# Optimization experiments

Measured on AMD Instinct MI355X. Metric: run time of the kernel, lower is better.

The kernel has to match this reference:

```python
import jax, jax.numpy as jnp
import numpy as np

D_MODEL = 2048
NUM_HEADS = 32
NUM_GROUPS = 8
D_K = D_MODEL // NUM_HEADS          # 64
GROUP_SIZE = NUM_HEADS // NUM_GROUPS  # 4


def setup_inputs() -> dict:
    key = jax.random.key(0)
    ks = jax.random.split(key, 7)
    B, S = 2, 2048
    x = jax.random.normal(ks[0], (B, S, D_MODEL), dtype=jnp.float32)
    sc = 1.0 / np.sqrt(D_MODEL)
    Wq = jax.random.normal(ks[1], (D_MODEL, D_MODEL), dtype=jnp.float32) * sc
    bq = jax.random.normal(ks[2], (D_MODEL,), dtype=jnp.float32) * 0.01
    Wk = jax.random.normal(ks[3], (D_MODEL, D_K * NUM_GROUPS), dtype=jnp.float32) * sc
    bk = jax.random.normal(ks[4], (D_K * NUM_GROUPS,), dtype=jnp.float32) * 0.01
    Wv = jax.random.normal(ks[5], (D_MODEL, D_K * NUM_GROUPS), dtype=jnp.float32) * sc
    bv = jax.random.normal(ks[6], (D_K * NUM_GROUPS,), dtype=jnp.float32) * 0.01
    return {"x": x, "Wq": Wq, "bq": bq, "Wk": Wk, "bk": bk, "Wv": Wv, "bv": bv}


def reference(x, Wq, bq, Wk, bk, Wv, bv):
    B, S, D = x.shape
    # q: (B, G, gs, S, dk)
    q = (x @ Wq + bq).reshape(B, S, NUM_HEADS, D_K).transpose(0, 2, 1, 3)
    q = q.reshape(B, NUM_GROUPS, GROUP_SIZE, S, D_K)
    # k, v: (B, G, S, dk)
    k = (x @ Wk + bk).reshape(B, S, NUM_GROUPS, D_K).transpose(0, 2, 1, 3)
    v = (x @ Wv + bv).reshape(B, S, NUM_GROUPS, D_K).transpose(0, 2, 1, 3)
    # scores: (B, G, gs, S_q, S_k)
    scores = jnp.einsum('bgqsd,bgtd->bgqst', q, k) / (D_K ** 0.5)
    attn = jax.nn.softmax(scores, axis=-1)
    out = jnp.einsum('bgqst,bgtd->bgqsd', attn, v)  # (B, G, gs, S, dk)
    # Faithful to source: transpose(1,2) then view(B, S, -1) (scrambles seq axis)
    out = out.transpose(0, 2, 1, 3, 4).reshape(B, S, -1)
    return out
```

## Files before the change

### kernel.cpp

```cpp
#include <hip/hip_runtime.h>

typedef _Float16 f16;
typedef _Float16 half8 __attribute__((ext_vector_type(8)));
typedef _Float16 half4v __attribute__((ext_vector_type(4)));
typedef __fp16 fp16x2 __attribute__((ext_vector_type(2)));
typedef float floatx4 __attribute__((ext_vector_type(4)));
typedef float f32x16 __attribute__((ext_vector_type(16)));
typedef unsigned uint4v __attribute__((ext_vector_type(4)));

#define GLL16(g, l) __builtin_amdgcn_global_load_lds( \
    (const __attribute__((address_space(1))) void*)(g), \
    (__attribute__((address_space(3))) void*)(l), 16, 0, 0)

static __device__ __forceinline__ float pairsum(float x) {
    return x + __shfl_xor(x, 32);
}
static __device__ __forceinline__ unsigned pkh(float a, float b) {
    fp16x2 h = __builtin_amdgcn_cvt_pkrtz(a, b);
    return __builtin_bit_cast(unsigned, h);
}

__global__ __launch_bounds__(256) void cvt_x_kernel(const float* __restrict__ x,
                                                    f16* __restrict__ xh) {
    size_t i = ((size_t)blockIdx.x * 256 + threadIdx.x) * 8;
    float4 a = *(const float4*)(x + i);
    float4 b = *(const float4*)(x + i + 4);
    half8 h;
    h[0] = (f16)a.x; h[1] = (f16)a.y; h[2] = (f16)a.z; h[3] = (f16)a.w;
    h[4] = (f16)b.x; h[5] = (f16)b.y; h[6] = (f16)b.z; h[7] = (f16)b.w;
    *(half8*)(xh + i) = h;
}

__global__ __launch_bounds__(256) void wt_kernel(const float* __restrict__ Wq,
                                                 const float* __restrict__ Wk,
                                                 const float* __restrict__ Wv,
                                                 f16* __restrict__ Wt) {
    __shared__ float tile[64][65];
    int n0 = (blockIdx.x % 48) * 64;
    int k0 = (blockIdx.x / 48) * 64;
    const float* src; int ld, c0;
    if (n0 < 2048)      { src = Wq; ld = 2048; c0 = n0; }
    else if (n0 < 2560) { src = Wk; ld = 512;  c0 = n0 - 2048; }
    else                { src = Wv; ld = 512;  c0 = n0 - 2560; }
    int t = threadIdx.x;
    #pragma unroll
    for (int i = 0; i < 16; ++i) {
        int idx = t + i * 256;
        int r = idx >> 6, c = idx & 63;
        tile[r][c] = src[(size_t)(k0 + r) * ld + c0 + c];
    }
    __syncthreads();
    #pragma unroll
    for (int i = 0; i < 2; ++i) {
        int idx = t + i * 256;
        int nr = idx >> 3, kc = (idx & 7) * 8;
        half8 h;
        #pragma unroll
        for (int j = 0; j < 8; ++j) h[j] = (f16)tile[kc + j][nr];
        *(half8*)(Wt + (size_t)(n0 + nr) * 2048 + k0 + kc) = h;
    }
}

__global__ __launch_bounds__(256) void qkv_gemm_kernel(
    const f16* __restrict__ A, const f16* __restrict__ Bt,
    const float* __restrict__ bq, const float* __restrict__ bk, const float* __restrict__ bv,
    f16* __restrict__ Qb, f16* __restrict__ Kb, f16* __restrict__ Vt) {
    __shared__ f16 As[128 * 64];
    __shared__ f16 Bs[128 * 64];
    const int K = 2048;
    int bid = blockIdx.x;
    int j5 = bid >> 3;
    int tm = (bid & 7) + 8 * (j5 / 24);
    int tn = j5 % 24;
    int m0 = tm * 128, n0 = tn * 128;
    int tid = threadIdx.x, lane = tid & 63, wid = tid >> 6;
    int wr = wid >> 1, wc = wid & 1;
    int lr = lane & 15, lg = lane >> 4;
    floatx4 acc[4][4] = {};

    int lrow = wid * 8 + (lane >> 3);
    int lcol = (((lane & 7) ^ ((lane >> 3) & 7)) * 8);
    char* AsB = (char*)As;
    char* BsB = (char*)Bs;
    int rsw = (lr & 7) << 4;

    for (int kt = 0; kt < K; kt += 64) {
        __syncthreads();
        #pragma unroll
        for (int i = 0; i < 4; ++i) {
            GLL16(A  + (size_t)(m0 + i * 32 + lrow) * K + kt + lcol, AsB + i * 4096 + wid * 1024);
            GLL16(Bt + (size_t)(n0 + i * 32 + lrow) * K + kt + lcol, BsB + i * 4096 + wid * 1024);
        }
        __syncthreads();
        #pragma unroll
        for (int ks = 0; ks < 2; ++ks) {
            half8 af[4], bf[4];
            #pragma unroll
            for (int i = 0; i < 4; ++i)
                af[i] = *(const half8*)(AsB + (wr * 64 + i * 16 + lr) * 128 + ((ks * 64 + lg * 16) ^ rsw));
            #pragma unroll
            for (int i = 0; i < 4; ++i)
                bf[i] = *(const half8*)(BsB + (wc * 64 + i * 16 + lr) * 128 + ((ks * 64 + lg * 16) ^ rsw));
            #pragma unroll
            for (int i = 0; i < 4; ++i)
                #pragma unroll
                for (int jj = 0; jj < 4; ++jj)
                    acc[i][jj] = __builtin_amdgcn_mfma_f32_16x16x32_f16(bf[jj], af[i], acc[i][jj], 0, 0, 0);
        }
    }

    int b = m0 >> 11;
    #pragma unroll
    for (int jj = 0; jj < 4; ++jj) {
        int nb = n0 + wc * 64 + jj * 16 + lg * 4;
        if (nb < 2048) {
            int hcol = nb >> 6, d0 = nb & 63;
            float4 bias4 = *(const float4*)(bq + nb);
            f16* dstb = Qb + (size_t)(b * 32 + hcol) * 131072 + d0;
            #pragma unroll
            for (int i = 0; i < 4; ++i) {
                int s = (m0 + wr * 64 + i * 16 + lr) & 2047;
                half4v hv;
                hv[0] = (f16)(acc[i][jj][0] + bias4.x);
                hv[1] = (f16)(acc[i][jj][1] + bias4.y);
                hv[2] = (f16)(acc[i][jj][2] + bias4.z);
                hv[3] = (f16)(acc[i][jj][3] + bias4.w);
                *(half4v*)(dstb + (size_t)s * 64) = hv;
            }
        } else if (nb < 2560) {
            int nk = nb - 2048;
            int gg = nk >> 6, d0 = nk & 63;
            float4 bias4 = *(const float4*)(bk + nk);
            f16* dstb = Kb + (size_t)(b * 8 + gg) * 131072 + d0;
            #pragma unroll
            for (int i = 0; i < 4; ++i) {
                int s = (m0 + wr * 64 + i * 16 + lr) & 2047;
                half4v hv;
                hv[0] = (f16)(acc[i][jj][0] + bias4.x);
                hv[1] = (f16)(acc[i][jj][1] + bias4.y);
                hv[2] = (f16)(acc[i][jj][2] + bias4.z);
                hv[3] = (f16)(acc[i][jj][3] + bias4.w);
                *(half4v*)(dstb + (size_t)s * 64) = hv;
            }
        } else {
            int nv = nb - 2560;
            int gg = nv >> 6, d0 = nv & 63;
            float4 bias4 = *(const float4*)(bv + nv);
            f16* dstb = Vt + (size_t)((b * 8 + gg) * 64 + d0) * 2048;
            #pragma unroll
            for (int i = 0; i < 4; ++i) {
                int s = (m0 + wr * 64 + i * 16 + lr) & 2047;
                int sp = (s & ~12) | ((s & 4) << 1) | ((s & 8) >> 1);
                dstb[sp]            = (f16)(acc[i][jj][0] + bias4.x);
                dstb[2048 + sp]     = (f16)(acc[i][jj][1] + bias4.y);
                dstb[4096 + sp]     = (f16)(acc[i][jj][2] + bias4.z);
                dstb[6144 + sp]     = (f16)(acc[i][jj][3] + bias4.w);
            }
        }
    }
}

__global__ __launch_bounds__(128, 2) void attn_kernel(
    const f16* __restrict__ Qb, const f16* __restrict__ Kb, const f16* __restrict__ Vt,
    float* __restrict__ out) {
    __shared__ __align__(16) f16 Kl[2][64 * 64];
    __shared__ __align__(16) f16 Vl[2][64 * 64];

    int bid = blockIdx.x;
    int hh = (bid & 7) * 8 + ((bid >> 3) & 7);
    int qb = bid >> 6;
    int b = hh >> 5, h = hh & 31, g = h >> 2, qh = h & 3;
    int tid = threadIdx.x, lane = tid & 63, wid = tid >> 6;
    int lc = lane & 31, hi = lane >> 5;

    const f16* Qhead = Qb + (size_t)(b * 32 + h) * 131072;
    const f16* Khead = Kb + (size_t)(b * 8 + g) * 131072;
    const f16* Vhead = Vt + (size_t)(b * 8 + g) * 131072;
    int q0 = qb * 128 + wid * 64;
    int sqA = q0 + lc, sqB = q0 + 32 + lc;

    half8 qfA[4], qfB[4];
    #pragma unroll
    for (int ks = 0; ks < 4; ++ks) {
        qfA[ks] = *(const half8*)(Qhead + (size_t)sqA * 64 + ks * 16 + hi * 8);
        qfB[ks] = *(const half8*)(Qhead + (size_t)sqB * 64 + ks * 16 + hi * 8);
    }

    f32x16 ocA0 = {}, ocA1 = {}, ocB0 = {}, ocB1 = {};
    float lA = 0.f, lB = 0.f;
    const float SC = 0.125f * 1.44269504088896f;
    const float MSH = 5.770780163555851f;

    int r_ = wid * 32 + (lane >> 3);
    int csx = ((lane & 7) ^ (r_ & 7)) * 8;
    char* KlB = (char*)Kl;
    char* VlB = (char*)Vl;

    int ro0 = lc * 128, ro1 = (lc + 32) * 128;
    int sw = (lc & 7) << 4;

    #pragma unroll
    for (int i = 0; i < 4; ++i) {
        GLL16(Khead + (size_t)(r_ + i * 8) * 64 + csx,        KlB + wid * 4096 + i * 1024);
        GLL16(Vhead + (size_t)(r_ + i * 8) * 2048 + csx,      VlB + wid * 4096 + i * 1024);
    }
    __syncthreads();

    #pragma unroll 1
    for (int t = 0; t < 32; ++t) {
        int c = t & 1;
        char* KB = KlB + c * 8192;
        char* VB = VlB + c * 8192;
        if (t < 31) {
            int nk = (t + 1) * 64;
            #pragma unroll
            for (int i = 0; i < 4; ++i) {
                GLL16(Khead + (size_t)(nk + r_ + i * 8) * 64 + csx,
                      KlB + (c ^ 1) * 8192 + wid * 4096 + i * 1024);
                GLL16(Vhead + (size_t)(r_ + i * 8) * 2048 + nk + csx,
                      VlB + (c ^ 1) * 8192 + wid * 4096 + i * 1024);
            }
        }

        f32x16 sA0 = {}, sA1 = {}, sB0 = {}, sB1 = {};
        __builtin_amdgcn_s_setprio(1);
        #pragma unroll
        for (int ks = 0; ks < 4; ++ks) {
            half8 kf0 = *(const half8*)(KB + ((ro0 + ks * 32 + hi * 16) ^ sw));
            half8 kf1 = *(const half8*)(KB + ((ro1 + ks * 32 + hi * 16) ^ sw));
            sA0 = __builtin_amdgcn_mfma_f32_32x32x16_f16(kf0, qfA[ks], sA0, 0, 0, 0);
            sA1 = __builtin_amdgcn_mfma_f32_32x32x16_f16(kf1, qfA[ks], sA1, 0, 0, 0);
            sB0 = __builtin_amdgcn_mfma_f32_32x32x16_f16(kf0, qfB[ks], sB0, 0, 0, 0);
            sB1 = __builtin_amdgcn_mfma_f32_32x32x16_f16(kf1, qfB[ks], sB1, 0, 0, 0);
        }
        __builtin_amdgcn_s_setprio(0);

        float rsA = 0.f, rsB = 0.f;
        #pragma unroll
        for (int r = 0; r < 16; ++r) {
            float pa0 = __builtin_amdgcn_exp2f(fmaf(sA0[r], SC, -MSH));
            float pa1 = __builtin_amdgcn_exp2f(fmaf(sA1[r], SC, -MSH));
            float pb0 = __builtin_amdgcn_exp2f(fmaf(sB0[r], SC, -MSH));
            float pb1 = __builtin_amdgcn_exp2f(fmaf(sB1[r], SC, -MSH));
            sA0[r] = pa0; sA1[r] = pa1; sB0[r] = pb0; sB1[r] = pb1;
            rsA += pa0 + pa1; rsB += pb0 + pb1;
        }
        lA += rsA; lB += rsB;

        #pragma unroll
        for (int tt = 0; tt < 2; ++tt) {
            #pragma unroll
            for (int ks2 = 0; ks2 < 2; ++ks2) {
                int base = ks2 * 8;
                uint4v uA, uB;
                if (tt == 0) {
                    uA[0] = pkh(sA0[base + 0], sA0[base + 1]);
                    uA[1] = pkh(sA0[base + 2], sA0[base + 3]);
                    uA[2] = pkh(sA0[base + 4], sA0[base + 5]);
                    uA[3] = pkh(sA0[base + 6], sA0[base + 7]);
                    uB[0] = pkh(sB0[base + 0], sB0[base + 1]);
                    uB[1] = pkh(sB0[base + 2], sB0[base + 3]);
                    uB[2] = pkh(sB0[base + 4], sB0[base + 5]);
                    uB[3] = pkh(sB0[base + 6], sB0[base + 7]);
                } else {
                    uA[0] = pkh(sA1[base + 0], sA1[base + 1]);
                    uA[1] = pkh(sA1[base + 2], sA1[base + 3]);
                    uA[2] = pkh(sA1[base + 4], sA1[base + 5]);
                    uA[3] = pkh(sA1[base + 6], sA1[base + 7]);
                    uB[0] = pkh(sB1[base + 0], sB1[base + 1]);
                    uB[1] = pkh(sB1[base + 2], sB1[base + 3]);
                    uB[2] = pkh(sB1[base + 4], sB1[base + 5]);
                    uB[3] = pkh(sB1[base + 6], sB1[base + 7]);
                }
                half8 pA = __builtin_bit_cast(half8, uA);
                half8 pB = __builtin_bit_cast(half8, uB);
                int cb = tt * 64 + ks2 * 32 + hi * 16;
                half8 vf0 = *(const half8*)(VB + ((ro0 + cb) ^ sw));
                half8 vf1 = *(const half8*)(VB + ((ro1 + cb) ^ sw));
                __builtin_amdgcn_s_setprio(1);
                ocA0 = __builtin_amdgcn_mfma_f32_32x32x16_f16(vf0, pA, ocA0, 0, 0, 0);
                ocA1 = __builtin_amdgcn_mfma_f32_32x32x16_f16(vf1, pA, ocA1, 0, 0, 0);
                ocB0 = __builtin_amdgcn_mfma_f32_32x32x16_f16(vf0, pB, ocB0, 0, 0, 0);
                ocB1 = __builtin_amdgcn_mfma_f32_32x32x16_f16(vf1, pB, ocB1, 0, 0, 0);
                __builtin_amdgcn_s_setprio(0);
            }
        }
        __syncthreads();
    }

    lA = pairsum(lA); lB = pairsum(lB);
    float invA = 1.f / lA, invB = 1.f / lB;
    size_t obase = (size_t)b * 4194304 + (size_t)(qh * 8 + g) * 131072 + hi * 4;
    size_t obA = obase + (size_t)sqA * 64;
    size_t obB = obase + (size_t)sqB * 64;
    #pragma unroll
    for (int rg = 0; rg < 4; ++rg) {
        floatx4 vA0, vA1, vB0, vB1;
        #pragma unroll
        for (int j = 0; j < 4; ++j) {
            vA0[j] = ocA0[rg * 4 + j] * invA;
            vA1[j] = ocA1[rg * 4 + j] * invA;
            vB0[j] = ocB0[rg * 4 + j] * invB;
            vB1[j] = ocB1[rg * 4 + j] * invB;
        }
        *(floatx4*)(out + obA + rg * 8) = vA0;
        *(floatx4*)(out + obA + 32 + rg * 8) = vA1;
        *(floatx4*)(out + obB + rg * 8) = vB0;
        *(floatx4*)(out + obB + 32 + rg * 8) = vB1;
    }
}

extern "C" void kernel_launch(void* const* d_in, const int* in_sizes, int n_in,
                              void* d_out, int out_size, void* d_ws, size_t ws_size,
                              hipStream_t stream) {
    const float* x  = (const float*)d_in[0];
    const float* Wq = (const float*)d_in[1];
    const float* bq = (const float*)d_in[2];
    const float* Wk = (const float*)d_in[3];
    const float* bk = (const float*)d_in[4];
    const float* Wv = (const float*)d_in[5];
    const float* bv = (const float*)d_in[6];
    float* out = (float*)d_out;

    char* ws = (char*)d_ws;
    f16* xh = (f16*)ws;
    f16* Wt = (f16*)(ws + 16777216);
    f16* Qb = (f16*)(ws + 29360128);
    f16* Kb = (f16*)(ws + 46137344);
    f16* Vt = (f16*)(ws + 50331648);

    cvt_x_kernel<<<4096, 256, 0, stream>>>(x, xh);
    wt_kernel<<<1536, 256, 0, stream>>>(Wq, Wk, Wv, Wt);
    qkv_gemm_kernel<<<768, 256, 0, stream>>>(xh, Wt, bq, bk, bv, Qb, Kb, Vt);
    attn_kernel<<<1024, 128, 0, stream>>>(Qb, Kb, Vt, out);
}
```

Baseline: 184.9 us.

## Software-pipeline attention: overlap next-tile QK MFMA with current softmax and PV

Restructures the attention main loop so the QK^T scores for tile t+1 are computed while tile t's softmax and P·V run, with K triple-buffered in LDS and prefetched two tiles ahead. The loop is unrolled by two and alternates between two score register sets. The aim is to hide exp/pack VALU latency behind MFMA work. The cost is extra registers for a second 64-value score set and extra LDS, which at 2 waves-per-EU launch bounds could cause spilling or lower occupancy.

```diff
diff --git a/kernel.cpp b/kernel.cpp
--- a/kernel.cpp
+++ b/kernel.cpp
@@ -18,6 +18,9 @@
 static __device__ __forceinline__ unsigned pkh(float a, float b) {
     fp16x2 h = __builtin_amdgcn_cvt_pkrtz(a, b);
     return __builtin_bit_cast(unsigned, h);
+}
+static __device__ __forceinline__ f32x16 mf(half8 a, half8 b, f32x16 c) {
+    return __builtin_amdgcn_mfma_f32_32x32x16_f16(a, b, c, 0, 0, 0);
 }
 
 __global__ __launch_bounds__(256) void cvt_x_kernel(const float* __restrict__ x,
@@ -160,10 +163,93 @@
     }
 }
 
+typedef struct { f32x16 a0, a1, b0, b1; } SS;
+
+static __device__ __forceinline__ void qk_step(const char* kR, int ro0, int ro1,
+        int sw, int hi, const half8 qfA[4], const half8 qfB[4], SS& S) {
+    f32x16 z = {};
+    S.a0 = z; S.a1 = z; S.b0 = z; S.b1 = z;
+    #pragma unroll
+    for (int ks = 0; ks < 4; ++ks) {
+        half8 kf0 = *(const half8*)(kR + ((ro0 + ks * 32 + hi * 16) ^ sw));
+        half8 kf1 = *(const half8*)(kR + ((ro1 + ks * 32 + hi * 16) ^ sw));
+        S.a0 = mf(kf0, qfA[ks], S.a0);
+        S.a1 = mf(kf1, qfA[ks], S.a1);
+        S.b0 = mf(kf0, qfB[ks], S.b0);
+        S.b1 = mf(kf1, qfB[ks], S.b1);
+    }
+}
+
+static __device__ __forceinline__ void sm_pack(SS& S, float& lA, float& lB,
+                                               uint4v PA[4], uint4v PB[4]) {
+    const float SC = 0.125f * 1.44269504088896f;
+    const float MSH = 5.770780163555851f;
+    float rsA = 0.f, rsB = 0.f;
+    #pragma unroll
+    for (int r = 0; r < 16; ++r) {
+        float a0 = __builtin_amdgcn_exp2f(fmaf(S.a0[r], SC, -MSH));
+        float a1 = __builtin_amdgcn_exp2f(fmaf(S.a1[r], SC, -MSH));
+        float b0 = __builtin_amdgcn_exp2f(fmaf(S.b0[r], SC, -MSH));
+        float b1 = __builtin_amdgcn_exp2f(fmaf(S.b1[r], SC, -MSH));
+        S.a0[r] = a0; S.a1[r] = a1; S.b0[r] = b0; S.b1[r] = b1;
+        rsA += a0 + a1; rsB += b0 + b1;
+    }
+    lA += rsA; lB += rsB;
+    #pragma unroll
+    for (int tt = 0; tt < 2; ++tt) {
+        #pragma unroll
+        for (int ks2 = 0; ks2 < 2; ++ks2) {
+            int base = ks2 * 8;
+            uint4v uA, uB;
+            if (tt == 0) {
+                uA[0] = pkh(S.a0[base + 0], S.a0[base + 1]);
+                uA[1] = pkh(S.a0[base + 2], S.a0[base + 3]);
+                uA[2] = pkh(S.a0[base + 4], S.a0[base + 5]);
+                uA[3] = pkh(S.a0[base + 6], S.a0[base + 7]);
+                uB[0] = pkh(S.b0[base + 0], S.b0[base + 1]);
+                uB[1] = pkh(S.b0[base + 2], S.b0[base + 3]);
+                uB[2] = pkh(S.b0[base + 4], S.b0[base + 5]);
+                uB[3] = pkh(S.b0[base + 6], S.b0[base + 7]);
+            } else {
+                uA[0] = pkh(S.a1[base + 0], S.a1[base + 1]);
+                uA[1] = pkh(S.a1[base + 2], S.a1[base + 3]);
+                uA[2] = pkh(S.a1[base + 4], S.a1[base + 5]);
+                uA[3] = pkh(S.a1[base + 6], S.a1[base + 7]);
+                uB[0] = pkh(S.b1[base + 0], S.b1[base + 1]);
+                uB[1] = pkh(S.b1[base + 2], S.b1[base + 3]);
+                uB[2] = pkh(S.b1[base + 4], S.b1[base + 5]);
+                uB[3] = pkh(S.b1[base + 6], S.b1[base + 7]);
+            }
+            PA[tt * 2 + ks2] = uA;
+            PB[tt * 2 + ks2] = uB;
+        }
+    }
+}
+
+static __device__ __forceinline__ void pv_step(const char* vR, int ro0, int ro1,
+        int sw, int hi, const uint4v PA[4], const uint4v PB[4],
+        f32x16& oA0, f32x16& oA1, f32x16& oB0, f32x16& oB1) {
+    #pragma unroll
+    for (int tt = 0; tt < 2; ++tt) {
+        #pragma unroll
+        for (int ks2 = 0; ks2 < 2; ++ks2) {
+            int cb = tt * 64 + ks2 * 32 + hi * 16;
+            half8 vf0 = *(const half8*)(vR + ((ro0 + cb) ^ sw));
+            half8 vf1 = *(const half8*)(vR + ((ro1 + cb) ^ sw));
+            half8 pA = __builtin_bit_cast(half8, PA[tt * 2 + ks2]);
+            half8 pB = __builtin_bit_cast(half8, PB[tt * 2 + ks2]);
+            oA0 = mf(vf0, pA, oA0);
+            oA1 = mf(vf1, pA, oA1);
+            oB0 = mf(vf0, pB, oB0);
+            oB1 = mf(vf1, pB, oB1);
+        }
+    }
+}
+
 __global__ __launch_bounds__(128, 2) void attn_kernel(
     const f16* __restrict__ Qb, const f16* __restrict__ Kb, const f16* __restrict__ Vt,
     float* __restrict__ out) {
-    __shared__ __align__(16) f16 Kl[2][64 * 64];
+    __shared__ __align__(16) f16 Kl[3][64 * 64];
     __shared__ __align__(16) f16 Vl[2][64 * 64];
 
     int bid = blockIdx.x;
@@ -188,105 +274,61 @@
 
     f32x16 ocA0 = {}, ocA1 = {}, ocB0 = {}, ocB1 = {};
     float lA = 0.f, lB = 0.f;
-    const float SC = 0.125f * 1.44269504088896f;
-    const float MSH = 5.770780163555851f;
 
     int r_ = wid * 32 + (lane >> 3);
     int csx = ((lane & 7) ^ (r_ & 7)) * 8;
     char* KlB = (char*)Kl;
     char* VlB = (char*)Vl;
-
     int ro0 = lc * 128, ro1 = (lc + 32) * 128;
     int sw = (lc & 7) << 4;
 
     #pragma unroll
     for (int i = 0; i < 4; ++i) {
-        GLL16(Khead + (size_t)(r_ + i * 8) * 64 + csx,        KlB + wid * 4096 + i * 1024);
-        GLL16(Vhead + (size_t)(r_ + i * 8) * 2048 + csx,      VlB + wid * 4096 + i * 1024);
+        GLL16(Khead + (size_t)(r_ + i * 8) * 64 + csx,       KlB + wid * 4096 + i * 1024);
+        GLL16(Khead + (size_t)(64 + r_ + i * 8) * 64 + csx,  KlB + 8192 + wid * 4096 + i * 1024);
+        GLL16(Vhead + (size_t)(r_ + i * 8) * 2048 + csx,     VlB + wid * 4096 + i * 1024);
     }
     __syncthreads();
 
+    char *kF = KlB, *kR = KlB + 8192, *kW = KlB + 16384;
+    char *vR = VlB, *vW = VlB + 8192;
+
+    SS Se, So;
+    qk_step(kF, ro0, ro1, sw, hi, qfA, qfB, Se);
+
+#define ATTN_HALF(SCUR, SNXT, T, QK_GUARD)                                        \
+    {                                                                             \
+        if ((T) < 30) {                                                           \
+            int nk2 = ((T) + 2) * 64;                                             \
+            _Pragma("unroll")                                                     \
+            for (int i = 0; i < 4; ++i)                                           \
+                GLL16(Khead + (size_t)(nk2 + r_ + i * 8) * 64 + csx,              \
+                      kW + wid * 4096 + i * 1024);                                \
+        }                                                                         \
+        if ((T) < 31) {                                                           \
+            int nk1 = ((T) + 1) * 64;                                             \
+            _Pragma("unroll")                                                     \
+            for (int i = 0; i < 4; ++i)                                           \
+                GLL16(Vhead + (size_t)(r_ + i * 8) * 2048 + nk1 + csx,            \
+                      vW + wid * 4096 + i * 1024);                                \
+        }                                                                         \
+        uint4v PA[4], PB[4];                                                      \
+        sm_pack(SCUR, lA, lB, PA, PB);                                            \
+        __builtin_amdgcn_s_setprio(1);                                            \
+        if (QK_GUARD) qk_step(kR, ro0, ro1, sw, hi, qfA, qfB, SNXT);              \
+        pv_step(vR, ro0, ro1, sw, hi, PA, PB, ocA0, ocA1, ocB0, ocB1);            \
+        __builtin_amdgcn_s_setprio(0);                                            \
+        __syncthreads();                                                          \
+        { char* _t = kF; kF = kR; kR = kW; kW = _t; }                             \
+        { char* _t = vR; vR = vW; vW = _t; }                                      \
+    }
+
     #pragma unroll 1
-    for (int t = 0; t < 32; ++t) {
-        int c = t & 1;
-        char* KB = KlB + c * 8192;
-        char* VB = VlB + c * 8192;
-        if (t < 31) {
-            int nk = (t + 1) * 64;
-            #pragma unroll
-            for (int i = 0; i < 4; ++i) {
-                GLL16(Khead + (size_t)(nk + r_ + i * 8) * 64 + csx,
-                      KlB + (c ^ 1) * 8192 + wid * 4096 + i * 1024);
-                GLL16(Vhead + (size_t)(r_ + i * 8) * 2048 + nk + csx,
-                      VlB + (c ^ 1) * 8192 + wid * 4096 + i * 1024);
-            }
-        }
-
-        f32x16 sA0 = {}, sA1 = {}, sB0 = {}, sB1 = {};
-        __builtin_amdgcn_s_setprio(1);
-        #pragma unroll
-        for (int ks = 0; ks < 4; ++ks) {
-            half8 kf0 = *(const half8*)(KB + ((ro0 + ks * 32 + hi * 16) ^ sw));
-            half8 kf1 = *(const half8*)(KB + ((ro1 + ks * 32 + hi * 16) ^ sw));
-            sA0 = __builtin_amdgcn_mfma_f32_32x32x16_f16(kf0, qfA[ks], sA0, 0, 0, 0);
-            sA1 = __builtin_amdgcn_mfma_f32_32x32x16_f16(kf1, qfA[ks], sA1, 0, 0, 0);
-            sB0 = __builtin_amdgcn_mfma_f32_32x32x16_f16(kf0, qfB[ks], sB0, 0, 0, 0);
-            sB1 = __builtin_amdgcn_mfma_f32_32x32x16_f16(kf1, qfB[ks], sB1, 0, 0, 0);
-        }
-        __builtin_amdgcn_s_setprio(0);
-
-        float rsA = 0.f, rsB = 0.f;
-        #pragma unroll
-        for (int r = 0; r < 16; ++r) {
-            float pa0 = __builtin_amdgcn_exp2f(fmaf(sA0[r], SC, -MSH));
-            float pa1 = __builtin_amdgcn_exp2f(fmaf(sA1[r], SC, -MSH));
-            float pb0 = __builtin_amdgcn_exp2f(fmaf(sB0[r], SC, -MSH));
-            float pb1 = __builtin_amdgcn_exp2f(fmaf(sB1[r], SC, -MSH));
-            sA0[r] = pa0; sA1[r] = pa1; sB0[r] = pb0; sB1[r] = pb1;
-            rsA += pa0 + pa1; rsB += pb0 + pb1;
-        }
-        lA += rsA; lB += rsB;
-
-        #pragma unroll
-        for (int tt = 0; tt < 2; ++tt) {
-            #pragma unroll
-            for (int ks2 = 0; ks2 < 2; ++ks2) {
-                int base = ks2 * 8;
-                uint4v uA, uB;
-                if (tt == 0) {
-                    uA[0] = pkh(sA0[base + 0], sA0[base + 1]);
-                    uA[1] = pkh(sA0[base + 2], sA0[base + 3]);
-                    uA[2] = pkh(sA0[base + 4], sA0[base + 5]);
-                    uA[3] = pkh(sA0[base + 6], sA0[base + 7]);
-                    uB[0] = pkh(sB0[base + 0], sB0[base + 1]);
-                    uB[1] = pkh(sB0[base + 2], sB0[base + 3]);
-                    uB[2] = pkh(sB0[base + 4], sB0[base + 5]);
-                    uB[3] = pkh(sB0[base + 6], sB0[base + 7]);
-                } else {
-                    uA[0] = pkh(sA1[base + 0], sA1[base + 1]);
-                    uA[1] = pkh(sA1[base + 2], sA1[base + 3]);
-                    uA[2] = pkh(sA1[base + 4], sA1[base + 5]);
-                    uA[3] = pkh(sA1[base + 6], sA1[base + 7]);
-                    uB[0] = pkh(sB1[base + 0], sB1[base + 1]);
-                    uB[1] = pkh(sB1[base + 2], sB1[base + 3]);
-                    uB[2] = pkh(sB1[base + 4], sB1[base + 5]);
-                    uB[3] = pkh(sB1[base + 6], sB1[base + 7]);
-                }
-                half8 pA = __builtin_bit_cast(half8, uA);
-                half8 pB = __builtin_bit_cast(half8, uB);
-                int cb = tt * 64 + ks2 * 32 + hi * 16;
-                half8 vf0 = *(const half8*)(VB + ((ro0 + cb) ^ sw));
-                half8 vf1 = *(const half8*)(VB + ((ro1 + cb) ^ sw));
-                __builtin_amdgcn_s_setprio(1);
-                ocA0 = __builtin_amdgcn_mfma_f32_32x32x16_f16(vf0, pA, ocA0, 0, 0, 0);
-                ocA1 = __builtin_amdgcn_mfma_f32_32x32x16_f16(vf1, pA, ocA1, 0, 0, 0);
-                ocB0 = __builtin_amdgcn_mfma_f32_32x32x16_f16(vf0, pB, ocB0, 0, 0, 0);
-                ocB1 = __builtin_amdgcn_mfma_f32_32x32x16_f16(vf1, pB, ocB1, 0, 0, 0);
-                __builtin_amdgcn_s_setprio(0);
-            }
-        }
-        __syncthreads();
-    }
+    for (int tb = 0; tb < 32; tb += 2) {
+        ATTN_HALF(Se, So, tb, true)
+        ATTN_HALF(So, Se, tb + 1, (tb + 1 < 31))
+    }
+#undef ATTN_HALF
 
     lA = pairsum(lA); lB = pairsum(lB);
     float invA = 1.f / lA, invB = 1.f / lB;
```

Measured after the change: 324.0 us. +75.2%, slower.
